# Kernel tuning notes

Hardware: AMD Instinct MI355X
Metric: run time of the kernel (lower is better)

## Reference

```python
import jax, jax.numpy as jnp
import numpy as np

B, S, D, H, DK, DV = 2, 2048, 1024, 16, 64, 64


def setup_inputs() -> dict:
    key = jax.random.key(0)
    ks = jax.random.split(key, 12)
    inp = {
        "query": jax.random.normal(ks[0], (B, S, D), jnp.float32),
        "key":   jax.random.normal(ks[1], (B, S, D), jnp.float32),
        "value": jax.random.normal(ks[2], (B, S, D), jnp.float32),
        # additive mask broadcast over per-head [B,S,S] scores (zeros = no masking)
        "mask":  jnp.zeros((S, S), jnp.float32),
        # stacked per-head projection params (math-equivalent to H separate Linears)
        "Wq": jax.random.normal(ks[3], (H, D, DK), jnp.float32) / np.sqrt(D),
        "bq": jax.random.normal(ks[4], (H, DK), jnp.float32) * 0.02,
        "Wk": jax.random.normal(ks[5], (H, D, DK), jnp.float32) / np.sqrt(D),
        "bk": jax.random.normal(ks[6], (H, DK), jnp.float32) * 0.02,
        "Wv": jax.random.normal(ks[7], (H, D, DV), jnp.float32) / np.sqrt(D),
        "bv": jax.random.normal(ks[8], (H, DV), jnp.float32) * 0.02,
        "Wo": jax.random.normal(ks[9], (H * DV, D), jnp.float32) / np.sqrt(H * DV),
        "bo": jax.random.normal(ks[10], (D,), jnp.float32) * 0.02,
    }
    return inp


def reference(query, key, value, mask, Wq, bq, Wk, bk, Wv, bv, Wo, bo):
    # per-head projections, vectorized over heads
    q = jnp.einsum("bsd,hdk->bhsk", query, Wq) + bq[None, :, None, :]
    k = jnp.einsum("bsd,hdk->bhsk", key, Wk) + bk[None, :, None, :]
    v = jnp.einsum("bsd,hdv->bhsv", value, Wv) + bv[None, :, None, :]
    # explicit QK^T softmax V, scale by sqrt(dim_k) (key.size(-1))
    scores = jnp.einsum("bhsk,bhtk->bhst", q, k) / jnp.sqrt(jnp.asarray(DK, q.dtype))
    scores = scores + mask  # broadcast [S,S] -> [B,H,S,S]
    attn = jax.nn.softmax(scores, axis=-1)
    out = jnp.einsum("bhst,bhtv->bhsv", attn, v)
    # concat heads along last dim: [B,S,H*DV]
    out = out.transpose(0, 2, 1, 3).reshape(B, S, H * DV)
    return out @ Wo + bo
```

## Files before the change

kernel.cpp:

```cpp
#include <hip/hip_runtime.h>
#include <stdint.h>

typedef __bf16 bf16;
typedef float f32x4 __attribute__((ext_vector_type(4)));
typedef __bf16 bf16x8 __attribute__((ext_vector_type(8)));
typedef __bf16 bf16x4 __attribute__((ext_vector_type(4)));
typedef __bf16 bf16x2 __attribute__((ext_vector_type(2)));
typedef unsigned u32x2 __attribute__((ext_vector_type(2)));
typedef unsigned u32x4 __attribute__((ext_vector_type(4)));

__device__ __forceinline__ void async_load16(const void* g, void* l) {
    __builtin_amdgcn_global_load_lds(
        (const __attribute__((address_space(1))) void*)g,
        (__attribute__((address_space(3))) void*)l, 16, 0, 0);
}

__device__ __forceinline__ unsigned pk2(float lo, float hi) {
    bf16x2 t;
    t[0] = (bf16)lo;
    t[1] = (bf16)hi;
    return __builtin_bit_cast(unsigned, t);
}

#if __has_builtin(__builtin_amdgcn_permlane32_swap)
#define PLSWAP32(A_, B_) do { u32x2 _r = __builtin_amdgcn_permlane32_swap((A_), (B_), false, false); (A_) = _r[0]; (B_) = _r[1]; } while (0)
#else
#define PLSWAP32(A_, B_) asm("v_permlane32_swap_b32 %0, %1" : "+v"(A_), "+v"(B_))
#endif
#if __has_builtin(__builtin_amdgcn_permlane16_swap)
#define PLSWAP16(A_, B_) do { u32x2 _r = __builtin_amdgcn_permlane16_swap((A_), (B_), false, false); (A_) = _r[0]; (B_) = _r[1]; } while (0)
#else
#define PLSWAP16(A_, B_) asm("v_permlane16_swap_b32 %0, %1" : "+v"(A_), "+v"(B_))
#endif

__global__ void detect_dtype(const unsigned short* __restrict__ q, int* __restrict__ flag) {
    __shared__ int cnt;
    if (threadIdx.x == 0) cnt = 0;
    __syncthreads();
    int c = 0;
    for (int i = threadIdx.x; i < 4096; i += 256) {
        int e = (q[i] >> 7) & 0xFF;
        if (e >= 0xC0) ++c;
    }
    atomicAdd(&cnt, c);
    __syncthreads();
    if (threadIdx.x == 0) { flag[0] = (cnt > 64) ? 1 : 0; flag[1] = 0; }
}

__global__ void prep(const void* __restrict__ qv, const void* __restrict__ vv,
                     const void* __restrict__ kvraw,
                     const void* __restrict__ wq, const void* __restrict__ wk,
                     const void* __restrict__ wv, const void* __restrict__ wo,
                     const unsigned int* __restrict__ mask,
                     bf16* __restrict__ Xq, bf16* __restrict__ Xv,
                     bf16* __restrict__ Xk,
                     bf16* __restrict__ WqT, bf16* __restrict__ WoT,
                     int* __restrict__ flag) {
    __shared__ bf16 t[32][33];
    const int f    = flag[0];
    const int task = blockIdx.z;
    const int bid  = blockIdx.x + 64 * blockIdx.y;

    if (task < 2) {
        const void* x = task ? vv : qv;
        bf16* o = task ? Xv : Xq;
        size_t i = ((size_t)bid * 256 + threadIdx.x) * 8;
        if (f) {
            f32x4 a = ((const f32x4*)x)[i / 4];
            f32x4 b = ((const f32x4*)x)[i / 4 + 1];
            bf16x8 v;
            for (int j = 0; j < 4; ++j) { v[j] = (bf16)a[j]; v[4 + j] = (bf16)b[j]; }
            *(bf16x8*)(o + i) = v;
        } else {
            *(bf16x8*)(o + i) = *(const bf16x8*)((const bf16*)x + i);
        }
    } else if (task < 5) {
        if (bid >= 1024) return;
        const void* in = (task == 2) ? wq : ((task == 3) ? wk : wv);
        int sub = bid >> 6, rem = bid & 63;
        int c0 = (rem & 1) * 32, r0 = (rem >> 1) * 32;
        int tx = threadIdx.x & 31, ty = threadIdx.x >> 5;
        size_t base = (size_t)sub * 65536;
        if (f) {
            const float* inF = (const float*)in;
            for (int i = 0; i < 32; i += 8)
                t[ty + i][tx] = (bf16)inF[base + (size_t)(r0 + ty + i) * 64 + (c0 + tx)];
        } else {
            const bf16* inB = (const bf16*)in;
            for (int i = 0; i < 32; i += 8)
                t[ty + i][tx] = inB[base + (size_t)(r0 + ty + i) * 64 + (c0 + tx)];
        }
        __syncthreads();
        bf16* o = WqT + ((size_t)(task - 2) * 16 + sub) * 65536;
        for (int i = 0; i < 32; i += 8)
            o[(size_t)(c0 + ty + i) * 1024 + (r0 + tx)] = t[tx][ty + i];
    } else if (task == 5) {
        if (bid >= 1024) return;
        int c0 = (bid & 31) * 32, r0 = (bid >> 5) * 32;
        int tx = threadIdx.x & 31, ty = threadIdx.x >> 5;
        if (f) {
            const float* inF = (const float*)wo;
            for (int i = 0; i < 32; i += 8)
                t[ty + i][tx] = (bf16)inF[(size_t)(r0 + ty + i) * 1024 + (c0 + tx)];
        } else {
            const bf16* inB = (const bf16*)wo;
            for (int i = 0; i < 32; i += 8)
                t[ty + i][tx] = inB[(size_t)(r0 + ty + i) * 1024 + (c0 + tx)];
        }
        __syncthreads();
        for (int i = 0; i < 32; i += 8)
            WoT[(size_t)(c0 + ty + i) * 1024 + (r0 + tx)] = t[tx][ty + i];
    } else if (task == 6) {
        const long nvec = (f ? 4194304L : 2097152L) / 4;
        unsigned int acc = 0;
        long stride = 2048L * 256;
        for (long i = (long)bid * 256 + threadIdx.x; i < nvec; i += stride) {
            uint4 v = ((const uint4*)mask)[i];
            acc |= v.x | v.y | v.z | v.w;
        }
        if (acc) atomicOr(flag + 1, 1);
    } else {
        if (!f) return;
        size_t i = ((size_t)bid * 256 + threadIdx.x) * 8;
        f32x4 a = ((const f32x4*)kvraw)[i / 4];
        f32x4 b2 = ((const f32x4*)kvraw)[i / 4 + 1];
        bf16x8 v;
        for (int j = 0; j < 4; ++j) { v[j] = (bf16)a[j]; v[4 + j] = (bf16)b2[j]; }
        *(bf16x8*)(Xk + i) = v;
    }
}

__global__ __launch_bounds__(256, 3) void gemm_qkv(
    const bf16* __restrict__ Xq, const void* __restrict__ keyRaw,
    const bf16* __restrict__ Xv, const bf16* __restrict__ Xk,
    const bf16* __restrict__ Bt,
    const void* __restrict__ b0, const void* __restrict__ b1, const void* __restrict__ b2,
    bf16* __restrict__ Qp, bf16* __restrict__ Kp, bf16* __restrict__ Vt,
    const int* __restrict__ flag, const int useXk) {
    __shared__ __attribute__((aligned(16))) unsigned char AsRaw[128 * 64 * 4];
    __shared__ __attribute__((aligned(16))) bf16 Bs[128 * 64];

    const int f = flag[0];
    const int K = 1024, N = 1024;
    const int z = blockIdx.z;
    const int af = (z == 1 && !useXk) ? f : 0;
    const void* Av = (z == 0) ? (const void*)Xq
                   : (z == 1) ? ((f && useXk) ? (const void*)Xk : keyRaw)
                              : (const void*)Xv;
    const void* bias = (z == 0) ? b0 : ((z == 1) ? b1 : b2);
    const bf16* B    = Bt + (size_t)z * 1024 * 1024;

    const int tid  = threadIdx.x;
    const int lane = tid & 63;
    const int w    = tid >> 6;
    const int quad = lane >> 4;
    const int mrow = lane & 15;
    const int m0 = blockIdx.y * 128;
    const int n0 = blockIdx.x * 128;
    const int wm = (w & 1) * 64;
    const int wn = (w >> 1) * 64;

    f32x4 acc[4][4] = {};

    for (int k0 = 0; k0 < K; k0 += 64) {
        if (af) {
            for (int it = 0; it < 8; ++it) {
                int ci  = it * 256 + tid;
                int row = ci >> 4, pc = ci & 15;
                int swz = ((row & 7) << 1) | ((row >> 3) & 1);
                int gc  = pc ^ swz;
                async_load16((const float*)Av + (size_t)(m0 + row) * K + k0 + gc * 4,
                             AsRaw + (size_t)(it * 256 + w * 64) * 16);
            }
        } else {
            for (int it = 0; it < 4; ++it) {
                int ci  = it * 256 + tid;
                int row = ci >> 3, pc = ci & 7;
                int gc  = pc ^ (row & 7);
                async_load16((const bf16*)Av + (size_t)(m0 + row) * K + k0 + gc * 8,
                             (bf16*)AsRaw + (size_t)(it * 256 + w * 64) * 8);
            }
        }
        for (int it = 0; it < 4; ++it) {
            int ci  = it * 256 + tid;
            int row = ci >> 3, pc = ci & 7;
            int gc  = pc ^ (row & 7);
            async_load16(B + (size_t)(n0 + row) * K + k0 + gc * 8,
                         Bs + (size_t)(it * 256 + w * 64) * 8);
        }
        __syncthreads();
        for (int kk = 0; kk < 2; ++kk) {
            bf16x8 afr[4], bfr[4];
            if (af) {
                const float* Asf = (const float*)AsRaw;
                for (int mi = 0; mi < 4; ++mi) {
                    int row = wm + mi * 16 + mrow;
                    int swz = ((row & 7) << 1) | ((row >> 3) & 1);
                    int lc  = (kk * 4 + quad) * 2;
                    f32x4 u0 = *(const f32x4*)(Asf + row * 64 + (lc ^ swz) * 4);
                    f32x4 u1 = *(const f32x4*)(Asf + row * 64 + ((lc + 1) ^ swz) * 4);
                    for (int j = 0; j < 4; ++j) {
                        afr[mi][j]     = (bf16)u0[j];
                        afr[mi][4 + j] = (bf16)u1[j];
                    }
                }
            } else {
                const bf16* Asb = (const bf16*)AsRaw;
                for (int mi = 0; mi < 4; ++mi) {
                    int row = wm + mi * 16 + mrow;
                    int pc  = (kk * 4 + quad) ^ (row & 7);
                    afr[mi] = *(const bf16x8*)(Asb + row * 64 + pc * 8);
                }
            }
            for (int ni = 0; ni < 4; ++ni) {
                int row = wn + ni * 16 + mrow;
                int pc  = (kk * 4 + quad) ^ (row & 7);
                bfr[ni] = *(const bf16x8*)(Bs + row * 64 + pc * 8);
            }
            for (int mi = 0; mi < 4; ++mi)
                for (int ni = 0; ni < 4; ++ni)
                    acc[mi][ni] = __builtin_amdgcn_mfma_f32_16x16x32_bf16(
                        afr[mi], bfr[ni], acc[mi][ni], 0, 0, 0);
        }
        __syncthreads();
    }

    const float scl = (z == 0) ? 0.18033688f : 1.0f;
    for (int ni = 0; ni < 4; ++ni) {
        int n    = n0 + wn + ni * 16 + mrow;
        float bv = f ? ((const float*)bias)[n] : (float)((const bf16*)bias)[n];
        for (int mi = 0; mi < 4; ++mi) {
            int mb = m0 + wm + mi * 16 + quad * 4;
            if (z == 2) {
                bf16x4 pk;
                for (int r = 0; r < 4; ++r) pk[r] = (bf16)(acc[mi][ni][r] + bv);
                *(bf16x4*)(Vt + (((size_t)(mb >> 11) * 1024 + n) << 11) + (mb & 2047)) = pk;
            } else {
                bf16* P = (z == 0) ? Qp : Kp;
                for (int r = 0; r < 4; ++r)
                    P[(size_t)(mb + r) * N + n] = (bf16)((acc[mi][ni][r] + bv) * scl);
            }
        }
    }
}

__global__ __launch_bounds__(256, 2) void gemm_out(
    const bf16* __restrict__ A, const bf16* __restrict__ Bt,
    const void* __restrict__ bias, void* __restrict__ Cout,
    const int* __restrict__ flag) {
    __shared__ __attribute__((aligned(16))) bf16 As[128 * 64];
    __shared__ __attribute__((aligned(16))) bf16 Bs[64 * 64];

    const int f = flag[0];
    const int K = 1024, N = 1024;
    const int tid  = threadIdx.x;
    const int lane = tid & 63;
    const int w    = tid >> 6;
    const int quad = lane >> 4;
    const int mrow = lane & 15;
    const int m0 = blockIdx.y * 128;
    const int n0 = blockIdx.x * 64;
    const int wm = (w & 1) * 64;
    const int wn = (w >> 1) * 32;

    f32x4 acc[4][2] = {};

    for (int k0 = 0; k0 < K; k0 += 64) {
        for (int it = 0; it < 4; ++it) {
            int ci  = it * 256 + tid;
            int row = ci >> 3, pc = ci & 7;
            int gc  = pc ^ (row & 7);
            async_load16(A + (size_t)(m0 + row) * K + k0 + gc * 8,
                         As + (size_t)(it * 256 + w * 64) * 8);
        }
        for (int it = 0; it < 2; ++it) {
            int ci  = it * 256 + tid;
            int row = ci >> 3, pc = ci & 7;
            int gc  = pc ^ (row & 7);
            async_load16(Bt + (size_t)(n0 + row) * K + k0 + gc * 8,
                         Bs + (size_t)(it * 256 + w * 64) * 8);
        }
        __syncthreads();
        for (int kk = 0; kk < 2; ++kk) {
            bf16x8 afr[4], bfr[2];
            for (int mi = 0; mi < 4; ++mi) {
                int row = wm + mi * 16 + mrow;
                int pc  = (kk * 4 + quad) ^ (row & 7);
                afr[mi] = *(const bf16x8*)(As + row * 64 + pc * 8);
            }
            for (int ni = 0; ni < 2; ++ni) {
                int row = wn + ni * 16 + mrow;
                int pc  = (kk * 4 + quad) ^ (row & 7);
                bfr[ni] = *(const bf16x8*)(Bs + row * 64 + pc * 8);
            }
            for (int mi = 0; mi < 4; ++mi)
                for (int ni = 0; ni < 2; ++ni)
                    acc[mi][ni] = __builtin_amdgcn_mfma_f32_16x16x32_bf16(
                        afr[mi], bfr[ni], acc[mi][ni], 0, 0, 0);
        }
        __syncthreads();
    }

    for (int ni = 0; ni < 2; ++ni) {
        int n    = n0 + wn + ni * 16 + mrow;
        float bv = f ? ((const float*)bias)[n] : (float)((const bf16*)bias)[n];
        for (int mi = 0; mi < 4; ++mi) {
            int mb = m0 + wm + mi * 16 + quad * 4;
            for (int r = 0; r < 4; ++r) {
                float val = acc[mi][ni][r] + bv;
                if (f) ((float*)Cout)[(size_t)(mb + r) * N + n] = val;
                else   ((bf16*)Cout)[(size_t)(mb + r) * N + n] = (bf16)val;
            }
        }
    }
}

__global__ __launch_bounds__(512, 4) void flash_attn(
    const bf16* __restrict__ Qp, const bf16* __restrict__ Kp,
    const bf16* __restrict__ Vt, const void* __restrict__ maskv,
    bf16* __restrict__ O, const int* __restrict__ flag) {
    __shared__ __attribute__((aligned(16))) bf16 Ks[2][4096];
    __shared__ __attribute__((aligned(16))) bf16 Vs[2][4096];

    const int f       = flag[0];
    const int useMask = flag[1];
    const int tid  = threadIdx.x;
    const int lane = tid & 63;
    const int w    = tid >> 6;
    const int quad = lane >> 4;
    const int c    = lane & 15;

    const int flat = blockIdx.x + 16 * (blockIdx.y + 16 * blockIdx.z);
    const int rx   = flat & 7;
    const int sx   = flat >> 3;
    const int pair = rx + 8 * (sx >> 4);
    const int s0   = (sx & 15) * 128;
    const int h    = pair & 15;
    const int b    = pair >> 4;

    const size_t qkBase = (size_t)b * 2048 * 1024 + h * 64;
    const size_t vtBase = ((size_t)b * 1024 + h * 64) * 2048;

    const int r0 = tid >> 3, g0 = (tid & 7) ^ (r0 & 7);
    const bf16* kp0 = Kp + qkBase + (size_t)r0 * 1024 + g0 * 8;
    const bf16* vp0 = Vt + vtBase + (size_t)r0 * 2048 + g0 * 8;

#define STAGE(B_, T_) do {                                                      \
        async_load16(kp0 + (size_t)(T_) * 1024, &Ks[B_][(size_t)(w * 64) * 8]); \
        async_load16(vp0 + (T_),                &Vs[B_][(size_t)(w * 64) * 8]); \
    } while (0)

    const bf16* kf0 = &Ks[0][c * 64 + ((0 + quad) ^ (c & 7)) * 8];
    const bf16* kf1 = &Ks[0][c * 64 + ((4 + quad) ^ (c & 7)) * 8];
    const bf16* vf0 = &Vs[0][c * 64 + ((0 + quad) ^ (c & 7)) * 8];
    const bf16* vf1 = &Vs[0][c * 64 + ((4 + quad) ^ (c & 7)) * 8];

    const bf16* qrow = Qp + qkBase + (size_t)(s0 + w * 16 + c) * 1024;
    bf16x8 aq0 = *(const bf16x8*)(qrow + quad * 8);
    bf16x8 aq1 = *(const bf16x8*)(qrow + 32 + quad * 8);

    u32x4 ou; ou[0] = 0x3F803F80u; ou[1] = 0x3F803F80u; ou[2] = 0x3F803F80u; ou[3] = 0x3F803F80u;
    const bf16x8 vones = __builtin_bit_cast(bf16x8, ou);

    f32x4 o_acc[4] = {};
    f32x4 o_l = {};

    const size_t mb0 = (size_t)(s0 + w * 16 + c) * 2048;

#define FCOMP(IB_, T_) do {                                                              \
        f32x4 sc[4] = {};                                                                \
        _Pragma("unroll") for (int tt = 0; tt < 4; ++tt) {                               \
            bf16x8 ak0 = *(const bf16x8*)(kf0 + (IB_) * 4096 + tt * 1024);               \
            bf16x8 ak1 = *(const bf16x8*)(kf1 + (IB_) * 4096 + tt * 1024);               \
            sc[tt] = __builtin_amdgcn_mfma_f32_16x16x32_bf16(ak0, aq0, sc[tt], 0, 0, 0); \
            sc[tt] = __builtin_amdgcn_mfma_f32_16x16x32_bf16(ak1, aq1, sc[tt], 0, 0, 0); \
        }                                                                                \
        if (useMask) {                                                                   \
            const size_t mr = mb0 + (T_);                                                \
            _Pragma("unroll") for (int tt = 0; tt < 4; ++tt) {                           \
                if (f) {                                                                 \
                    f32x4 mk = *(const f32x4*)((const float*)maskv + mr + tt * 16 + quad * 4); \
                    for (int r = 0; r < 4; ++r) sc[tt][r] += mk[r] * 1.44269504f;        \
                } else {                                                                 \
                    bf16x4 mk = *(const bf16x4*)((const bf16*)maskv + mr + tt * 16 + quad * 4); \
                    for (int r = 0; r < 4; ++r) sc[tt][r] += (float)mk[r] * 1.44269504f; \
                }                                                                        \
            }                                                                            \
        }                                                                                \
        unsigned Wp[4][2];                                                               \
        _Pragma("unroll") for (int tt = 0; tt < 4; ++tt) {                               \
            Wp[tt][0] = pk2(exp2f(sc[tt][0]), exp2f(sc[tt][1]));                         \
            Wp[tt][1] = pk2(exp2f(sc[tt][2]), exp2f(sc[tt][3]));                         \
        }                                                                                \
        _Pragma("unroll") for (int kk = 0; kk < 2; ++kk) {                               \
            unsigned a0 = Wp[2 * kk][0], b0v = Wp[2 * kk + 1][0];                        \
            unsigned a1 = Wp[2 * kk][1], b1v = Wp[2 * kk + 1][1];                        \
            PLSWAP32(a0, b0v);                                                           \
            PLSWAP16(a0, b0v);                                                           \
            PLSWAP32(a1, b1v);                                                           \
            PLSWAP16(a1, b1v);                                                           \
            u32x4 uv; uv[0] = a0; uv[1] = a1; uv[2] = b0v; uv[3] = b1v;                  \
            bf16x8 ap = __builtin_bit_cast(bf16x8, uv);                                  \
            const bf16* vfb = kk ? vf1 : vf0;                                            \
            _Pragma("unroll") for (int ni = 0; ni < 4; ++ni) {                           \
                bf16x8 bv = *(const bf16x8*)(vfb + (IB_) * 4096 + ni * 1024);            \
                o_acc[ni] = __builtin_amdgcn_mfma_f32_16x16x32_bf16(ap, bv, o_acc[ni], 0, 0, 0); \
            }                                                                            \
            o_l = __builtin_amdgcn_mfma_f32_16x16x32_bf16(ap, vones, o_l, 0, 0, 0);      \
        }                                                                                \
    } while (0)

    STAGE(0, 0);
    for (int t0 = 0; t0 < 2048; t0 += 128) {
        __syncthreads();
        STAGE(1, t0 + 64);
        FCOMP(0, t0);
        __syncthreads();
        if (t0 + 128 < 2048) STAGE(0, t0 + 128);
        FCOMP(1, t0 + 64);
    }
#undef STAGE
#undef FCOMP

    for (int r = 0; r < 4; ++r) {
        float inv = 1.0f / o_l[r];
        size_t roff = (size_t)(b * 2048 + s0 + w * 16 + quad * 4 + r) * 1024 + h * 64;
        for (int ni = 0; ni < 4; ++ni)
            O[roff + ni * 16 + c] = (bf16)(o_acc[ni][r] * inv);
    }
}

extern "C" void kernel_launch(void* const* d_in, const int* in_sizes, int n_in,
                              void* d_out, int out_size, void* d_ws, size_t ws_size,
                              hipStream_t stream) {
    bf16* ws = (bf16*)d_ws;
    (void)in_sizes; (void)n_in; (void)out_size;

    const size_t MM = 1024 * 1024;
    int*  flag = (int*)ws;
    bf16* WqT  = ws + 8;
    bf16* WoT  = WqT + 3 * MM;
    bf16* Qp   = WoT + MM;
    bf16* Kp   = Qp + 4 * MM;
    bf16* Xq   = Kp + 4 * MM;
    bf16* AO   = Xq;
    bf16* Xk   = Xq + 4 * MM;
    bf16* Xv   = (bf16*)d_out;
    bf16* Vt   = (bf16*)d_out + 4 * MM;

    const int useXk = (ws_size >= (size_t)(20 * MM) * sizeof(bf16) + 16) ? 1 : 0;

    detect_dtype<<<1, 256, 0, stream>>>((const unsigned short*)d_in[0], flag);

    prep<<<dim3(64, 32, useXk ? 8 : 7), 256, 0, stream>>>(
        d_in[0], d_in[2], d_in[1], d_in[4], d_in[6], d_in[8], d_in[10],
        (const unsigned int*)d_in[3], Xq, Xv, Xk, WqT, WoT, flag);

    gemm_qkv<<<dim3(8, 32, 3), 256, 0, stream>>>(Xq, d_in[1], Xv, Xk, WqT,
                                                 d_in[5], d_in[7], d_in[9],
                                                 Qp, Kp, Vt, flag, useXk);

    flash_attn<<<dim3(16, 16, 2), 512, 0, stream>>>(Qp, Kp, Vt, d_in[3], AO, flag);

    gemm_out<<<dim3(16, 32, 1), 256, 0, stream>>>(AO, WoT, d_in[11], d_out, flag);
}
```

Measured before the change: 267.9 us.

## Swizzle GEMM block order and compute softmax row sums with VALU instead of MFMA

Both projection GEMMs remap the flat block index so groups of 8 consecutive workgroups share the same N column tile across different M rows, which is meant to improve L2 reuse of the weight tiles. The attention kernel drops the extra MFMA against a ones vector that accumulated the softmax denominator. It now sums the fp32 exponentials per lane, reduces them with cross-lane shuffles at the end, and broadcasts the per-row sum. This removes one MFMA per 32-key chunk but adds VALU adds. The sum now uses fp32 values rather than the bf16-rounded weights used for P·V, which slightly changes numerics.

```diff
diff --git a/kernel.cpp b/kernel.cpp
--- a/kernel.cpp
+++ b/kernel.cpp
@@ -142,7 +142,15 @@
 
     const int f = flag[0];
     const int K = 1024, N = 1024;
-    const int z = blockIdx.z;
+
+    const int flat = blockIdx.x + 8 * blockIdx.y + 256 * blockIdx.z;
+    const int rxw  = flat & 7;
+    const int sxw  = flat >> 3;
+    const int xb   = sxw & 7;
+    const int jb   = sxw >> 3;
+    const int yb   = rxw + 8 * (jb & 3);
+    const int z    = jb >> 2;
+
     const int af = (z == 1 && !useXk) ? f : 0;
     const void* Av = (z == 0) ? (const void*)Xq
                    : (z == 1) ? ((f && useXk) ? (const void*)Xk : keyRaw)
@@ -155,8 +163,8 @@
     const int w    = tid >> 6;
     const int quad = lane >> 4;
     const int mrow = lane & 15;
-    const int m0 = blockIdx.y * 128;
-    const int n0 = blockIdx.x * 128;
+    const int m0 = yb * 128;
+    const int n0 = xb * 128;
     const int wm = (w & 1) * 64;
     const int wn = (w >> 1) * 64;
 
@@ -258,8 +266,15 @@
     const int w    = tid >> 6;
     const int quad = lane >> 4;
     const int mrow = lane & 15;
-    const int m0 = blockIdx.y * 128;
-    const int n0 = blockIdx.x * 64;
+
+    const int flat = blockIdx.x + 16 * blockIdx.y;
+    const int rxw  = flat & 7;
+    const int sxw  = flat >> 3;
+    const int xb   = sxw & 15;
+    const int yb   = rxw + 8 * (sxw >> 4);
+
+    const int m0 = yb * 128;
+    const int n0 = xb * 64;
     const int wm = (w & 1) * 64;
     const int wn = (w >> 1) * 32;
 
@@ -359,11 +374,8 @@
     bf16x8 aq0 = *(const bf16x8*)(qrow + quad * 8);
     bf16x8 aq1 = *(const bf16x8*)(qrow + 32 + quad * 8);
 
-    u32x4 ou; ou[0] = 0x3F803F80u; ou[1] = 0x3F803F80u; ou[2] = 0x3F803F80u; ou[3] = 0x3F803F80u;
-    const bf16x8 vones = __builtin_bit_cast(bf16x8, ou);
-
     f32x4 o_acc[4] = {};
-    f32x4 o_l = {};
+    float l_s = 0.f;
 
     const size_t mb0 = (size_t)(s0 + w * 16 + c) * 2048;
 
@@ -388,9 +400,16 @@
             }                                                                            \
         }                                                                                \
         unsigned Wp[4][2];                                                               \
-        _Pragma("unroll") for (int tt = 0; tt < 4; ++tt) {                               \
-            Wp[tt][0] = pk2(exp2f(sc[tt][0]), exp2f(sc[tt][1]));                         \
-            Wp[tt][1] = pk2(exp2f(sc[tt][2]), exp2f(sc[tt][3]));                         \
+        {                                                                                \
+            float rsum = 0.f;                                                            \
+            _Pragma("unroll") for (int tt = 0; tt < 4; ++tt) {                           \
+                float p0 = exp2f(sc[tt][0]), p1 = exp2f(sc[tt][1]);                      \
+                float p2 = exp2f(sc[tt][2]), p3 = exp2f(sc[tt][3]);                      \
+                rsum += (p0 + p1) + (p2 + p3);                                           \
+                Wp[tt][0] = pk2(p0, p1);                                                 \
+                Wp[tt][1] = pk2(p2, p3);                                                 \
+            }                                                                            \
+            l_s += rsum;                                                                 \
         }                                                                                \
         _Pragma("unroll") for (int kk = 0; kk < 2; ++kk) {                               \
             unsigned a0 = Wp[2 * kk][0], b0v = Wp[2 * kk + 1][0];                        \
@@ -406,7 +425,6 @@
                 bf16x8 bv = *(const bf16x8*)(vfb + (IB_) * 4096 + ni * 1024);            \
                 o_acc[ni] = __builtin_amdgcn_mfma_f32_16x16x32_bf16(ap, bv, o_acc[ni], 0, 0, 0); \
             }                                                                            \
-            o_l = __builtin_amdgcn_mfma_f32_16x16x32_bf16(ap, vones, o_l, 0, 0, 0);      \
         }                                                                                \
     } while (0)
 
@@ -422,11 +440,17 @@
 #undef STAGE
 #undef FCOMP
 
-    for (int r = 0; r < 4; ++r) {
-        float inv = 1.0f / o_l[r];
-        size_t roff = (size_t)(b * 2048 + s0 + w * 16 + quad * 4 + r) * 1024 + h * 64;
-        for (int ni = 0; ni < 4; ++ni)
-            O[roff + ni * 16 + c] = (bf16)(o_acc[ni][r] * inv);
+    {
+        float ls = l_s;
+        ls += __shfl_xor(ls, 16, 64);
+        ls += __shfl_xor(ls, 32, 64);
+        for (int r = 0; r < 4; ++r) {
+            float lv   = __shfl(ls, quad * 4 + r, 64);
+            float inv  = 1.0f / lv;
+            size_t roff = (size_t)(b * 2048 + s0 + w * 16 + quad * 4 + r) * 1024 + h * 64;
+            for (int ni = 0; ni < 4; ++ni)
+                O[roff + ni * 16 + c] = (bf16)(o_acc[ni][r] * inv);
+        }
     }
 }
 
```

New measurement: 258.5 us (median of 2 runs). 1.04x faster.
